# Performance work log

Hardware: AMD Instinct MI355X
Metric: run time of the kernel (lower is better)

The kernel has to match this reference:

```python
import jax, jax.numpy as jnp
import numpy as np

B, K, D, FD = 4096, 200, 128, 1024  # batch, neighbors, embed dim, item_fields*D
MASK_FILL = -(2.0 ** 32) + 1.0


def setup_inputs() -> dict:
    key = jax.random.key(0)
    k1, k2, k3, k4, k5 = jax.random.split(key, 5)
    target_feats = jax.random.normal(k1, (B, FD), dtype=jnp.float32)
    neighbor_feats = jax.random.normal(k2, (B, K, D), dtype=jnp.float32)
    neighbor_label = jax.random.normal(k3, (B, K, D), dtype=jnp.float32)
    hist_mask = jax.random.randint(k4, (B, K), 0, 2, dtype=jnp.int32)
    # Linear(item_fields*D -> D, bias=False): weight shape (out, in) = (D, FD)
    limit = float(np.sqrt(6.0 / (D + FD)))  # xavier_uniform
    W = jax.random.uniform(k5, (D, FD), dtype=jnp.float32, minval=-limit, maxval=limit)
    return {"target_feats": target_feats, "neighbor_feats": neighbor_feats,
            "neighbor_label": neighbor_label, "hist_mask": hist_mask, "W": W}


def reference(target_feats, neighbor_feats, neighbor_label, hist_mask, W):
    # target = self.W(target_feats): [B, D]
    target = jnp.einsum('bf,df->bd', target_feats, W)
    # alpha = matmul(neighbor_feats, target[..., None]).squeeze(): [B, K]
    alpha = jnp.einsum('bkd,bd->bk', neighbor_feats, target)
    alpha = jnp.where(hist_mask > 0, alpha, MASK_FILL)
    alpha = jax.nn.softmax(alpha, axis=1)  # [B, K]
    neighbor_embd = jnp.einsum('bk,bkd->bd', alpha, neighbor_feats)
    label_embd = jnp.einsum('bk,bkd->bd', alpha, neighbor_label)
    return (neighbor_embd, label_embd)
```

## Files before the change

kernel.cpp:

```cpp
#include <hip/hip_runtime.h>
#include <math.h>

#define BB   4096
#define KK   200
#define DD   128
#define FDIM 1024
#define MASK_FILL (-4294967295.0f)

typedef float fx4 __attribute__((ext_vector_type(4)));

__global__ __launch_bounds__(256) void target_gemm(const float* __restrict__ tf,
                                                   const float* __restrict__ W,
                                                   float* __restrict__ tgt) {
    __shared__ float s_tf[8 * FDIM];
    __shared__ float s_red[8][DD];
    const int tid = threadIdx.x;
    const int d   = tid & 127;
    const int h   = tid >> 7;
    const size_t r0 = (size_t)blockIdx.x * 8;

    const fx4* src = (const fx4*)(tf + r0 * FDIM);
    for (int i = tid; i < 8 * FDIM / 4; i += 256)
        ((fx4*)s_tf)[i] = src[i];
    __syncthreads();

    float acc[8] = {0, 0, 0, 0, 0, 0, 0, 0};
    const fx4* wr = (const fx4*)(W + (size_t)d * FDIM) + h * (FDIM / 8);
    #pragma unroll 4
    for (int i = 0; i < FDIM / 8; ++i) {
        fx4 w = wr[i];
        #pragma unroll
        for (int r = 0; r < 8; ++r) {
            fx4 t = ((const fx4*)(s_tf + r * FDIM + h * (FDIM / 2)))[i];
            acc[r] += w.x * t.x + w.y * t.y + w.z * t.z + w.w * t.w;
        }
    }
    if (h == 1) {
        #pragma unroll
        for (int r = 0; r < 8; ++r) s_red[r][d] = acc[r];
    }
    __syncthreads();
    if (h == 0) {
        #pragma unroll
        for (int r = 0; r < 8; ++r)
            tgt[(r0 + r) * DD + d] = acc[r] + s_red[r][d];
    }
}

__global__ __launch_bounds__(256) void attn_online(const float* __restrict__ nf,
                                                   const float* __restrict__ nl,
                                                   const int*   __restrict__ mask,
                                                   const float* __restrict__ tgt,
                                                   float* __restrict__ out) {
    const int tid  = threadIdx.x;
    const int lane = tid & 63;
    const int l32  = lane & 31;
    const int h    = (lane >> 5) & 1;
    const int b    = __builtin_amdgcn_readfirstlane(blockIdx.x * 4 + (tid >> 6));

    const fx4* nf4 = (const fx4*)(nf + (size_t)b * KK * DD);
    const fx4* nl4 = (const fx4*)(nl + (size_t)b * KK * DD);
    const int* mb  = mask + (size_t)b * KK;
    const fx4  tg  = ((const fx4*)(tgt + (size_t)b * DD))[l32];

    float m = -INFINITY, s = 0.0f;
    fx4 an = {0, 0, 0, 0}, al = {0, 0, 0, 0};

    for (int c = 0; c < 20; ++c) {
        fx4 vn[5], vl[5];
        #pragma unroll
        for (int j = 0; j < 5; ++j) {
            const int idx = (c * 5 + j) * 64 + lane;
            vn[j] = __builtin_nontemporal_load(nf4 + idx);
            vl[j] = __builtin_nontemporal_load(nl4 + idx);
        }
        float a[5];
        #pragma unroll
        for (int j = 0; j < 5; ++j) {
            float d = vn[j].x * tg.x + vn[j].y * tg.y + vn[j].z * tg.z + vn[j].w * tg.w;
            #pragma unroll
            for (int off = 16; off > 0; off >>= 1)
                d += __shfl_xor(d, off);
            const int k0 = (c * 5 + j) * 2;
            const int mk = h ? mb[k0 + 1] : mb[k0];
            a[j] = (mk > 0) ? d : MASK_FILL;
        }
        const float mc = fmaxf(fmaxf(fmaxf(a[0], a[1]), fmaxf(a[2], a[3])), a[4]);
        const float mn = fmaxf(m, mc);
        const float r  = __expf(m - mn);
        m = mn;
        s *= r; an *= r; al *= r;
        #pragma unroll
        for (int j = 0; j < 5; ++j) {
            const float p = __expf(a[j] - m);
            s  += p;
            an += p * vn[j];
            al += p * vl[j];
        }
    }

    const float mo = __shfl_xor(m, 32);
    const float so = __shfl_xor(s, 32);
    fx4 ano, alo;
    ano.x = __shfl_xor(an.x, 32); ano.y = __shfl_xor(an.y, 32);
    ano.z = __shfl_xor(an.z, 32); ano.w = __shfl_xor(an.w, 32);
    alo.x = __shfl_xor(al.x, 32); alo.y = __shfl_xor(al.y, 32);
    alo.z = __shfl_xor(al.z, 32); alo.w = __shfl_xor(al.w, 32);
    const float mt  = fmaxf(m, mo);
    const float eL  = __expf(m - mt);
    const float eO  = __expf(mo - mt);
    const float inv = 1.0f / (s * eL + so * eO);

    if (h == 0) {
        fx4 r = (an * eL + ano * eO) * inv;
        __builtin_nontemporal_store(r, &((fx4*)(out + (size_t)b * DD))[l32]);
    } else {
        fx4 r = (al * eL + alo * eO) * inv;
        __builtin_nontemporal_store(r, &((fx4*)(out + (size_t)BB * DD + (size_t)b * DD))[l32]);
    }
}

extern "C" void kernel_launch(void* const* d_in, const int* in_sizes, int n_in,
                              void* d_out, int out_size, void* d_ws, size_t ws_size,
                              hipStream_t stream) {
    const float* tf   = (const float*)d_in[0];
    const float* nf   = (const float*)d_in[1];
    const float* nl   = (const float*)d_in[2];
    const int*   mask = (const int*)d_in[3];
    const float* W    = (const float*)d_in[4];
    float* out = (float*)d_out;
    float* tgt = (float*)d_ws;

    target_gemm<<<BB / 8, 256, 0, stream>>>(tf, W, tgt);
    attn_online<<<BB / 4, 256, 0, stream>>>(nf, nl, mask, tgt, out);
}
```

Measured before the change: 185.3 us.

## Split each batch row's neighbor loop across two waves with LDS merge

Each batch row is now handled by two wavefronts, each covering half of the 200 neighbors. The two online-softmax partial states are merged through shared memory after a block barrier. The per-iteration register tile shrinks from 5 to 2 vectors and launch bounds request higher occupancy. The aim is more waves in flight to hide memory latency on this bandwidth-bound kernel. In exchange it adds a __syncthreads, LDS traffic and an extra merge step, and leaves fewer loads in flight per wave.

```diff
diff --git a/kernel.cpp b/kernel.cpp
--- a/kernel.cpp
+++ b/kernel.cpp
@@ -47,51 +47,56 @@
     }
 }
 
-__global__ __launch_bounds__(256) void attn_online(const float* __restrict__ nf,
-                                                   const float* __restrict__ nl,
-                                                   const int*   __restrict__ mask,
-                                                   const float* __restrict__ tgt,
-                                                   float* __restrict__ out) {
+__global__ __launch_bounds__(256, 8) void attn_online(const float* __restrict__ nf,
+                                                      const float* __restrict__ nl,
+                                                      const int*   __restrict__ mask,
+                                                      const float* __restrict__ tgt,
+                                                      float* __restrict__ out) {
+    __shared__ float s_m[2][2], s_s[2][2];
+    __shared__ fx4   s_an[2][2][32];
+    __shared__ fx4   s_al[2][2][32];
+
     const int tid  = threadIdx.x;
     const int lane = tid & 63;
     const int l32  = lane & 31;
     const int h    = (lane >> 5) & 1;
-    const int b    = __builtin_amdgcn_readfirstlane(blockIdx.x * 4 + (tid >> 6));
+    const int bloc = tid >> 7;
+    const int b    = __builtin_amdgcn_readfirstlane(blockIdx.x * 2 + bloc);
+    const int w    = __builtin_amdgcn_readfirstlane((tid >> 6) & 1);
 
-    const fx4* nf4 = (const fx4*)(nf + (size_t)b * KK * DD);
-    const fx4* nl4 = (const fx4*)(nl + (size_t)b * KK * DD);
-    const int* mb  = mask + (size_t)b * KK;
+    const fx4* nf4 = (const fx4*)(nf + (size_t)b * KK * DD) + (size_t)w * 50 * 64;
+    const fx4* nl4 = (const fx4*)(nl + (size_t)b * KK * DD) + (size_t)w * 50 * 64;
+    const int* mb  = mask + (size_t)b * KK + w * 100;
     const fx4  tg  = ((const fx4*)(tgt + (size_t)b * DD))[l32];
 
     float m = -INFINITY, s = 0.0f;
     fx4 an = {0, 0, 0, 0}, al = {0, 0, 0, 0};
 
-    for (int c = 0; c < 20; ++c) {
-        fx4 vn[5], vl[5];
+    for (int c = 0; c < 25; ++c) {
+        fx4 vn[2], vl[2];
         #pragma unroll
-        for (int j = 0; j < 5; ++j) {
-            const int idx = (c * 5 + j) * 64 + lane;
+        for (int j = 0; j < 2; ++j) {
+            const int idx = (c * 2 + j) * 64 + lane;
             vn[j] = __builtin_nontemporal_load(nf4 + idx);
             vl[j] = __builtin_nontemporal_load(nl4 + idx);
         }
-        float a[5];
+        float a[2];
         #pragma unroll
-        for (int j = 0; j < 5; ++j) {
+        for (int j = 0; j < 2; ++j) {
             float d = vn[j].x * tg.x + vn[j].y * tg.y + vn[j].z * tg.z + vn[j].w * tg.w;
             #pragma unroll
             for (int off = 16; off > 0; off >>= 1)
                 d += __shfl_xor(d, off);
-            const int k0 = (c * 5 + j) * 2;
+            const int k0 = c * 4 + 2 * j;
             const int mk = h ? mb[k0 + 1] : mb[k0];
             a[j] = (mk > 0) ? d : MASK_FILL;
         }
-        const float mc = fmaxf(fmaxf(fmaxf(a[0], a[1]), fmaxf(a[2], a[3])), a[4]);
-        const float mn = fmaxf(m, mc);
+        const float mn = fmaxf(m, fmaxf(a[0], a[1]));
         const float r  = __expf(m - mn);
         m = mn;
         s *= r; an *= r; al *= r;
         #pragma unroll
-        for (int j = 0; j < 5; ++j) {
+        for (int j = 0; j < 2; ++j) {
             const float p = __expf(a[j] - m);
             s  += p;
             an += p * vn[j];
@@ -99,24 +104,41 @@
         }
     }
 
-    const float mo = __shfl_xor(m, 32);
-    const float so = __shfl_xor(s, 32);
-    fx4 ano, alo;
-    ano.x = __shfl_xor(an.x, 32); ano.y = __shfl_xor(an.y, 32);
-    ano.z = __shfl_xor(an.z, 32); ano.w = __shfl_xor(an.w, 32);
-    alo.x = __shfl_xor(al.x, 32); alo.y = __shfl_xor(al.y, 32);
-    alo.z = __shfl_xor(al.z, 32); alo.w = __shfl_xor(al.w, 32);
-    const float mt  = fmaxf(m, mo);
-    const float eL  = __expf(m - mt);
-    const float eO  = __expf(mo - mt);
-    const float inv = 1.0f / (s * eL + so * eO);
+    {
+        const float mo = __shfl_xor(m, 32);
+        const float so = __shfl_xor(s, 32);
+        fx4 ano, alo;
+        ano.x = __shfl_xor(an.x, 32); ano.y = __shfl_xor(an.y, 32);
+        ano.z = __shfl_xor(an.z, 32); ano.w = __shfl_xor(an.w, 32);
+        alo.x = __shfl_xor(al.x, 32); alo.y = __shfl_xor(al.y, 32);
+        alo.z = __shfl_xor(al.z, 32); alo.w = __shfl_xor(al.w, 32);
+        const float mt = fmaxf(m, mo);
+        const float e0 = __expf(m - mt);
+        const float e1 = __expf(mo - mt);
+        s  = s * e0 + so * e1;
+        an = an * e0 + ano * e1;
+        al = al * e0 + alo * e1;
+        m  = mt;
+    }
 
-    if (h == 0) {
-        fx4 r = (an * eL + ano * eO) * inv;
-        __builtin_nontemporal_store(r, &((fx4*)(out + (size_t)b * DD))[l32]);
-    } else {
-        fx4 r = (al * eL + alo * eO) * inv;
-        __builtin_nontemporal_store(r, &((fx4*)(out + (size_t)BB * DD + (size_t)b * DD))[l32]);
+    if (h == 0) s_an[bloc][w][l32] = an; else s_al[bloc][w][l32] = al;
+    if (lane == 0) { s_m[bloc][w] = m; s_s[bloc][w] = s; }
+    __syncthreads();
+
+    if (w == 0) {
+        const float m1 = s_m[bloc][1];
+        const float s1 = s_s[bloc][1];
+        const fx4 mine  = (h == 0) ? an : al;
+        const fx4 other = (h == 0) ? s_an[bloc][1][l32] : s_al[bloc][1][l32];
+        const float M   = fmaxf(m, m1);
+        const float e0  = __expf(m - M);
+        const float e1  = __expf(m1 - M);
+        const float inv = 1.0f / (s * e0 + s1 * e1);
+        const fx4 r = (mine * e0 + other * e1) * inv;
+        if (h == 0)
+            __builtin_nontemporal_store(r, &((fx4*)(out + (size_t)b * DD))[l32]);
+        else
+            __builtin_nontemporal_store(r, &((fx4*)(out + (size_t)BB * DD + (size_t)b * DD))[l32]);
     }
 }
 
@@ -132,5 +154,5 @@
     float* tgt = (float*)d_ws;
 
     target_gemm<<<BB / 8, 256, 0, stream>>>(tf, W, tgt);
-    attn_online<<<BB / 4, 256, 0, stream>>>(nf, nl, mask, tgt, out);
+    attn_online<<<BB / 2, 256, 0, stream>>>(nf, nl, mask, tgt, out);
 }
```

Result: faster. 173.5 us (-6.4%).
